# Kernel tuning notes

Measured on AMD Instinct MI355X. Metric: run time of the kernel, lower is better.

## Reference

```python
import jax, jax.numpy as jnp
import numpy as np

N = 200000      # nodes (1000 graphs x 200 nodes)
E = 1600000     # edges
N1 = 100000     # nodes after pool 1
E2 = 100000     # edges of pooled graph
N2 = 50000      # nodes after pool 2
B = 1000        # graphs
F_IN, C1, C2, H, NCLS = 1, 32, 64, 25, 10


def setup_inputs() -> dict:
    key = jax.random.key(0)
    ks = jax.random.split(key, 16)
    def lin(k, i, o):
        return jax.random.normal(k, (i, o), jnp.float32) / np.sqrt(i)
    inp = {
        'x': jax.random.normal(ks[0], (N, F_IN), jnp.float32),
        'pos': jax.random.uniform(ks[1], (N, 2), jnp.float32),
        'edge_index': jax.random.randint(ks[2], (2, E), 0, N, dtype=jnp.int32),
        'edge_attr': jax.random.uniform(ks[3], (E, 2), jnp.float32),
        'batch': (jnp.arange(N, dtype=jnp.int32) // (N // B)),
        'cluster1': (jnp.arange(N, dtype=jnp.int32) // 2),      # pairs of consecutive nodes -> same graph
        'edge_index2': jax.random.randint(ks[4], (2, E2), 0, N1, dtype=jnp.int32),
        'cluster2': (jnp.arange(N1, dtype=jnp.int32) // 2),
        'n1_w1': lin(ks[5], 2, H), 'n1_b1': jnp.zeros((H,), jnp.float32),
        'n1_w2': lin(ks[6], H, F_IN * C1), 'n1_b2': jnp.zeros((F_IN * C1,), jnp.float32),
        'root1': lin(ks[7], F_IN, C1), 'bias1': jnp.zeros((C1,), jnp.float32),
        'n2_w1': lin(ks[8], 2, H), 'n2_b1': jnp.zeros((H,), jnp.float32),
        'n2_w2': lin(ks[9], H, C1 * C2), 'n2_b2': jnp.zeros((C1 * C2,), jnp.float32),
        'root2': lin(ks[10], C1, C2), 'bias2': jnp.zeros((C2,), jnp.float32),
        'fc1_w': lin(ks[11], C2, 128), 'fc1_b': jnp.zeros((128,), jnp.float32),
        'fc2_w': lin(ks[12], 128, NCLS), 'fc2_b': jnp.zeros((NCLS,), jnp.float32),
    }
    return inp


def _cartesian(ei, pos):
    # PyG transforms.Cartesian(norm=True, cat=False)
    cart = pos[ei[0]] - pos[ei[1]]                      # [E, 2]
    m = jnp.max(jnp.abs(cart))
    return cart / (2.0 * m) + 0.5


def _nnconv(x, ei, ea, w1, b1, w2, b2, root, bias, n_nodes, c_in, c_out):
    # edge-conditioned weights: MLP(edge_attr) -> [E, c_in, c_out]
    w = (jax.nn.relu(ea @ w1 + b1) @ w2 + b2).reshape(-1, c_in, c_out)
    msg = jnp.einsum('ei,eio->eo', x[ei[0]], w)          # per-edge matmul with gathered src feats
    agg = jax.ops.segment_sum(msg, ei[1], num_segments=n_nodes)
    return agg + x @ root + bias


def _segment_mean(v, seg, n):
    s = jax.ops.segment_sum(v, seg, num_segments=n)
    c = jax.ops.segment_sum(jnp.ones((v.shape[0], 1), v.dtype), seg, num_segments=n)
    return s / jnp.maximum(c, 1.0)


def reference(x, pos, edge_index, edge_attr, batch, cluster1, edge_index2, cluster2,
              n1_w1, n1_b1, n1_w2, n1_b2, root1, bias1,
              n2_w1, n2_b1, n2_w2, n2_b2, root2, bias2,
              fc1_w, fc1_b, fc2_w, fc2_b):
    h = jax.nn.elu(_nnconv(x, edge_index, edge_attr, n1_w1, n1_b1, n1_w2, n1_b2,
                           root1, bias1, N, F_IN, C1))
    # max_pool(cluster1): segment-max feats, mean pos, carry batch; recompute Cartesian attrs
    x1 = jax.ops.segment_max(h, cluster1, num_segments=N1)
    pos1 = _segment_mean(pos, cluster1, N1)
    batch1 = jax.ops.segment_max(batch, cluster1, num_segments=N1)
    ea2 = _cartesian(edge_index2, pos1)
    h2 = jax.nn.elu(_nnconv(x1, edge_index2, ea2, n2_w1, n2_b1, n2_w2, n2_b2,
                            root2, bias2, N1, C1, C2))
    # max_pool_x(cluster2)
    x2 = jax.ops.segment_max(h2, cluster2, num_segments=N2)
    batch2 = jax.ops.segment_max(batch1, cluster2, num_segments=N2)
    g = _segment_mean(x2, batch2, B)                    # global_mean_pool -> [B, 64]
    z = jax.nn.elu(g @ fc1_w + fc1_b)                   # dropout is identity in eval
    return jax.nn.log_softmax(z @ fc2_w + fc2_b, axis=1)
```

## Files before the change

kernel.cpp:

```cpp
#include <hip/hip_runtime.h>
#include <hip/hip_bf16.h>

#define N_NODES 200000
#define E1 1600000
#define N1P 100000
#define E2P 100000
#define N2P 50000
#define BGR 1000
#define C1 32
#define C2 64
#define HIDN 25
#define NCLS 10

typedef short short8 __attribute__((ext_vector_type(8)));
typedef int int4v __attribute__((ext_vector_type(4)));
typedef float f32x4 __attribute__((ext_vector_type(4)));
typedef float f32x2 __attribute__((ext_vector_type(2)));

union FragU { int4v i; short8 s; };

__device__ __forceinline__ float elu1(float v) {
    return v > 0.f ? v : expm1f(v);
}
__device__ __forceinline__ float bf2f(unsigned short u) {
    return __uint_as_float(((unsigned int)u) << 16);
}
__device__ __forceinline__ unsigned int pk_bf16(float a, float b) {
    unsigned int r;
    asm("v_cvt_pk_bf16_f32 %0, %1, %2" : "=v"(r) : "v"(a), "v"(b));
    return r;
}
__device__ __forceinline__ void atomic_pk_bf16(unsigned short* p, unsigned int pk) {
    asm volatile("global_atomic_pk_add_bf16 %0, %1, off" :: "v"(p), "v"(pk) : "memory");
}

__global__ __launch_bounds__(256) void bgbuild1_kernel(
    const float* __restrict__ w2, const float* __restrict__ b2,
    unsigned int* __restrict__ W2f)
{
    int q = blockIdx.x * 256 + threadIdx.x;
    if (q >= 512) return;
    int jj = q & 3, l = (q >> 2) & 63, m = q >> 8;
    int k0 = (l >> 4) * 8 + 2 * jj;
    int o = 2 * (l & 15) + m;
    float v0 = (k0 < 25) ? w2[k0 * 32 + o] : (k0 == 25 ? b2[o] : 0.f);
    int k1 = k0 + 1;
    float v1 = (k1 < 25) ? w2[k1 * 32 + o] : (k1 == 25 ? b2[o] : 0.f);
    W2f[q] = pk_bf16(v0, v1);
}

__global__ __launch_bounds__(256) void conv1_kernel(
    const float* __restrict__ x, const float* __restrict__ ea,
    const int* __restrict__ ei,
    const float* __restrict__ w1, const float* __restrict__ b1,
    const unsigned int* __restrict__ W2f,
    unsigned short* __restrict__ agg1b)
{
    __shared__ unsigned int afrag[16][4][64];
    __shared__ int dst_lds[256];

    int t = threadIdx.x;
    int e = blockIdx.x * 256 + t;
    f32x2 a = ((const f32x2*)ea)[e];
    int s = ei[e], d = ei[E1 + e];
    float xv = x[s];
    dst_lds[t] = d;

    float v[26];
#pragma unroll
    for (int h = 0; h < HIDN; ++h) {
        float u = fmaf(a.x, w1[h], fmaf(a.y, w1[HIDN + h], b1[h]));
        v[h] = fmaxf(u, 0.f) * xv;
    }
    v[25] = xv;

    int tile = t >> 4, r = t & 15;
#pragma unroll
    for (int p = 0; p < 13; ++p) {
        int g = p >> 2, j = p & 3;
        afrag[tile][j][g * 16 + r] = pk_bf16(v[2 * p], v[2 * p + 1]);
    }
    afrag[tile][1][48 + r] = 0;
    afrag[tile][2][48 + r] = 0;
    afrag[tile][3][48 + r] = 0;
    __syncthreads();

    int lane = t & 63, wave = t >> 6;
    FragU bf0, bf1;
    bf0.i = *(const int4v*)(W2f + lane * 4);
    bf1.i = *(const int4v*)(W2f + (64 + lane) * 4);
    int c = lane & 15, rg = lane >> 4;

#pragma unroll
    for (int ti = 0; ti < 4; ++ti) {
        int tl = wave * 4 + ti;
        FragU af;
        af.i.x = afrag[tl][0][lane];
        af.i.y = afrag[tl][1][lane];
        af.i.z = afrag[tl][2][lane];
        af.i.w = afrag[tl][3][lane];
        f32x4 a0 = (f32x4){0.f, 0.f, 0.f, 0.f};
        f32x4 a1 = (f32x4){0.f, 0.f, 0.f, 0.f};
        a0 = __builtin_amdgcn_mfma_f32_16x16x32_bf16(af.s, bf0.s, a0, 0, 0, 0);
        a1 = __builtin_amdgcn_mfma_f32_16x16x32_bf16(af.s, bf1.s, a1, 0, 0, 0);
#pragma unroll
        for (int jj = 0; jj < 4; ++jj) {
            int le = tl * 16 + rg * 4 + jj;
            atomic_pk_bf16(agg1b + (size_t)dst_lds[le] * C1 + 2 * c,
                           pk_bf16(a0[jj], a1[jj]));
        }
    }
}

__global__ __launch_bounds__(256) void pool1_kernel(
    const unsigned short* __restrict__ agg1b, const float* __restrict__ x,
    const float* __restrict__ root1, const float* __restrict__ bias1,
    const float* __restrict__ pos, unsigned short* __restrict__ x1b,
    float* __restrict__ pos1)
{
    int t = blockIdx.x * blockDim.x + threadIdx.x;
    if (t >= N1P * C1) return;
    int j = t >> 5, o = t & 31;
    int na = 2 * j, nb = 2 * j + 1;
    float r = root1[o], bo = bias1[o];
    float ha = elu1(bf2f(agg1b[(size_t)na * C1 + o]) + x[na] * r + bo);
    float hb = elu1(bf2f(agg1b[(size_t)nb * C1 + o]) + x[nb] * r + bo);
    float mx = fmaxf(ha, hb);
    x1b[t] = (unsigned short)(pk_bf16(mx, mx) & 0xffffu);
    if (o < 2) pos1[j * 2 + o] = 0.5f * (pos[na * 2 + o] + pos[nb * 2 + o]);
}

__global__ __launch_bounds__(256) void maxabs_kernel(
    const int* __restrict__ ei2, const float* __restrict__ pos1,
    unsigned int* __restrict__ maxbits)
{
    int e = blockIdx.x * blockDim.x + threadIdx.x;
    float m = 0.f;
    if (e < E2P) {
        int s = ei2[e], d = ei2[E2P + e];
        float c0 = pos1[2 * s] - pos1[2 * d];
        float c1 = pos1[2 * s + 1] - pos1[2 * d + 1];
        m = fmaxf(fabsf(c0), fabsf(c1));
    }
#pragma unroll
    for (int off = 32; off; off >>= 1)
        m = fmaxf(m, __shfl_down(m, off));
    if ((threadIdx.x & 63) == 0)
        atomicMax(maxbits, __float_as_uint(m));
}

__global__ __launch_bounds__(256) void bgbuild_kernel(
    const float* __restrict__ w2, const float* __restrict__ b2,
    unsigned int* __restrict__ Bg)
{
    int idx = blockIdx.x * 256 + threadIdx.x;
    if (idx >= 26 * 4 * 64 * 4) return;
    int g0 = idx * 2;
    int j = g0 & 7;
    int l = (g0 >> 3) & 63;
    int nb = (g0 >> 9) & 3;
    int kt = g0 >> 11;
    int k = kt * 32 + (l >> 4) * 8 + j;
    int o = (nb >> 1) * 32 + 2 * (l & 15) + (nb & 1);
    float v0, v1;
    if (k < 800) { v0 = w2[k * 64 + o]; v1 = w2[(k + 1) * 64 + o]; }
    else         { v0 = b2[(k - 800) * 64 + o]; v1 = b2[(k - 799) * 64 + o]; }
    Bg[idx] = pk_bf16(v0, v1);
}

__global__ __launch_bounds__(256) void conv2_kernel(
    const int* __restrict__ ei2, const float* __restrict__ pos1,
    const unsigned short* __restrict__ x1b,
    const float* __restrict__ w1, const float* __restrict__ b1,
    const unsigned int* __restrict__ maxbits,
    const unsigned int* __restrict__ Bg,
    unsigned short* __restrict__ agg2b)
{
    __shared__ __align__(16) unsigned short xs_lds[256][40];
    __shared__ float hid_lds[256][27];
    __shared__ int dst_lds[256];

    int t = threadIdx.x;
    int ge = blockIdx.x * 256 + t;

    {
        float inv = 0.5f / __uint_as_float(maxbits[0]);
        int s = 0, d = 0;
        if (ge < E2P) { s = ei2[ge]; d = ei2[E2P + ge]; }
        dst_lds[t] = d;
        float a0 = (pos1[2 * s] - pos1[2 * d]) * inv + 0.5f;
        float a1 = (pos1[2 * s + 1] - pos1[2 * d + 1]) * inv + 0.5f;
#pragma unroll
        for (int h = 0; h < HIDN; ++h) {
            float u = fmaf(a0, w1[h], fmaf(a1, w1[HIDN + h], b1[h]));
            hid_lds[t][h] = fmaxf(u, 0.f);
        }
        const int4v* xp = (const int4v*)(x1b + (size_t)s * C1);
#pragma unroll
        for (int q = 0; q < 4; ++q)
            *(int4v*)&xs_lds[t][q * 8] = xp[q];
    }
    __syncthreads();

    int lane = t & 63, wave = t >> 6;
    int c = lane & 15, rg = lane >> 4;

    FragU xv4[4];
    float xfl[4][8];
#pragma unroll
    for (int ti = 0; ti < 4; ++ti) {
        int row = (wave * 4 + ti) * 16 + c;
        xv4[ti].i = *(const int4v*)&xs_lds[row][rg * 8];
#pragma unroll
        for (int g2 = 0; g2 < 4; ++g2) {
            unsigned int u = (unsigned int)xv4[ti].i[g2];
            xfl[ti][2 * g2]     = __uint_as_float(u << 16);
            xfl[ti][2 * g2 + 1] = __uint_as_float(u & 0xffff0000u);
        }
    }

    f32x4 acc[4][4];
#pragma unroll
    for (int ti = 0; ti < 4; ++ti)
#pragma unroll
        for (int nb = 0; nb < 4; ++nb)
            acc[ti][nb] = (f32x4){0.f, 0.f, 0.f, 0.f};

    const int4v* Bg4 = (const int4v*)Bg;
#pragma unroll 2
    for (int kt = 0; kt < 25; ++kt) {
        FragU bf[4];
#pragma unroll
        for (int nb = 0; nb < 4; ++nb)
            bf[nb].i = Bg4[(kt * 4 + nb) * 64 + lane];
#pragma unroll
        for (int ti = 0; ti < 4; ++ti) {
            float hv = hid_lds[(wave * 4 + ti) * 16 + c][kt];
            FragU af;
            af.i.x = pk_bf16(hv * xfl[ti][0], hv * xfl[ti][1]);
            af.i.y = pk_bf16(hv * xfl[ti][2], hv * xfl[ti][3]);
            af.i.z = pk_bf16(hv * xfl[ti][4], hv * xfl[ti][5]);
            af.i.w = pk_bf16(hv * xfl[ti][6], hv * xfl[ti][7]);
#pragma unroll
            for (int nb = 0; nb < 4; ++nb)
                acc[ti][nb] = __builtin_amdgcn_mfma_f32_16x16x32_bf16(af.s, bf[nb].s, acc[ti][nb], 0, 0, 0);
        }
    }
    {
        FragU bf[4];
#pragma unroll
        for (int nb = 0; nb < 4; ++nb)
            bf[nb].i = Bg4[(25 * 4 + nb) * 64 + lane];
#pragma unroll
        for (int ti = 0; ti < 4; ++ti)
#pragma unroll
            for (int nb = 0; nb < 4; ++nb)
                acc[ti][nb] = __builtin_amdgcn_mfma_f32_16x16x32_bf16(xv4[ti].s, bf[nb].s, acc[ti][nb], 0, 0, 0);
    }

#pragma unroll
    for (int ti = 0; ti < 4; ++ti) {
        int tl = wave * 4 + ti;
#pragma unroll
        for (int jj = 0; jj < 4; ++jj) {
            int le = tl * 16 + rg * 4 + jj;
            if (blockIdx.x * 256 + le < E2P) {
                unsigned short* dp = agg2b + (size_t)dst_lds[le] * C2;
                atomic_pk_bf16(dp + 2 * c,      pk_bf16(acc[ti][0][jj], acc[ti][1][jj]));
                atomic_pk_bf16(dp + 32 + 2 * c, pk_bf16(acc[ti][2][jj], acc[ti][3][jj]));
            }
        }
    }
}

__global__ __launch_bounds__(256) void pool2_kernel(
    const unsigned short* __restrict__ agg2b, const unsigned short* __restrict__ x1b,
    const float* __restrict__ root2, const float* __restrict__ bias2,
    float* __restrict__ g)
{
    int b = blockIdx.x;
    int w = threadIdx.x >> 6, o = threadIdx.x & 63;
    __shared__ float part[4][C2];
    float sum = 0.f;
    for (int jj = w; jj < 50; jj += 4) {
        int j = b * 50 + jj;
        float hv[2];
#pragma unroll
        for (int t = 0; t < 2; ++t) {
            int n = 2 * j + t;
            float a = bf2f(agg2b[(size_t)n * C2 + o]) + bias2[o];
#pragma unroll
            for (int i = 0; i < C1; ++i)
                a = fmaf(bf2f(x1b[(size_t)n * C1 + i]), root2[i * C2 + o], a);
            hv[t] = elu1(a);
        }
        sum += fmaxf(hv[0], hv[1]);
    }
    part[w][o] = sum;
    __syncthreads();
    if (w == 0) {
        float s2 = part[0][o] + part[1][o] + part[2][o] + part[3][o];
        g[b * C2 + o] = s2 * (1.f / 50.f);
    }
}

__global__ __launch_bounds__(128) void head_kernel(
    const float* __restrict__ g,
    const float* __restrict__ fc1w, const float* __restrict__ fc1b,
    const float* __restrict__ fc2w, const float* __restrict__ fc2b,
    float* __restrict__ out)
{
    int b = blockIdx.x;
    int t = threadIdx.x;
    __shared__ float gs[C2];
    __shared__ float zs[128];
    __shared__ float ls[NCLS];
    if (t < C2) gs[t] = g[b * C2 + t];
    __syncthreads();
    float z = fc1b[t];
#pragma unroll
    for (int i = 0; i < C2; ++i) z = fmaf(gs[i], fc1w[i * 128 + t], z);
    zs[t] = elu1(z);
    __syncthreads();
    if (t < NCLS) {
        float l = fc2b[t];
#pragma unroll
        for (int k = 0; k < 128; ++k) l = fmaf(zs[k], fc2w[k * NCLS + t], l);
        ls[t] = l;
    }
    __syncthreads();
    if (t < NCLS) {
        float mx = ls[0];
#pragma unroll
        for (int c = 1; c < NCLS; ++c) mx = fmaxf(mx, ls[c]);
        float se = 0.f;
#pragma unroll
        for (int c = 0; c < NCLS; ++c) se += expf(ls[c] - mx);
        out[b * NCLS + t] = ls[t] - mx - logf(se);
    }
}

extern "C" void kernel_launch(void* const* d_in, const int* in_sizes, int n_in,
                              void* d_out, int out_size, void* d_ws, size_t ws_size,
                              hipStream_t stream)
{
    const float* x    = (const float*)d_in[0];
    const float* pos  = (const float*)d_in[1];
    const int*   ei   = (const int*)d_in[2];
    const float* ea   = (const float*)d_in[3];
    const int*   ei2  = (const int*)d_in[6];
    const float* n1w1 = (const float*)d_in[8];
    const float* n1b1 = (const float*)d_in[9];
    const float* n1w2 = (const float*)d_in[10];
    const float* n1b2 = (const float*)d_in[11];
    const float* root1= (const float*)d_in[12];
    const float* bias1= (const float*)d_in[13];
    const float* n2w1 = (const float*)d_in[14];
    const float* n2b1 = (const float*)d_in[15];
    const float* n2w2 = (const float*)d_in[16];
    const float* n2b2 = (const float*)d_in[17];
    const float* root2= (const float*)d_in[18];
    const float* bias2= (const float*)d_in[19];
    const float* fc1w = (const float*)d_in[20];
    const float* fc1b = (const float*)d_in[21];
    const float* fc2w = (const float*)d_in[22];
    const float* fc2b = (const float*)d_in[23];
    float* out = (float*)d_out;

    char* w = (char*)d_ws;
    unsigned short* agg1b = (unsigned short*)w;  w += (size_t)N_NODES * C1 * 2;
    unsigned short* x1b   = (unsigned short*)w;  w += (size_t)N1P * C1 * 2;
    float* pos1 = (float*)w;                     w += (size_t)N1P * 2 * 4;
    unsigned int* maxbits = (unsigned int*)w;    w += 256;
    unsigned short* agg2b = (unsigned short*)w;  w += (size_t)N1P * C2 * 2;
    float* g    = (float*)w;                     w += (size_t)BGR * C2 * 4;
    unsigned int* Bg = (unsigned int*)w;         w += 26624 * 4;
    unsigned int* W2f = (unsigned int*)w;        w += 512 * 4;

    hipMemsetAsync(agg1b, 0, (size_t)N_NODES * C1 * 2, stream);
    hipMemsetAsync(agg2b, 0, (size_t)N1P * C2 * 2, stream);
    hipMemsetAsync(maxbits, 0, 256, stream);

    bgbuild1_kernel<<<2, 256, 0, stream>>>(n1w2, n1b2, W2f);
    bgbuild_kernel<<<104, 256, 0, stream>>>(n2w2, n2b2, Bg);
    conv1_kernel<<<E1 / 256, 256, 0, stream>>>(x, ea, ei, n1w1, n1b1, W2f, agg1b);
    pool1_kernel<<<(N1P * C1 + 255) / 256, 256, 0, stream>>>(agg1b, x, root1, bias1, pos, x1b, pos1);
    maxabs_kernel<<<(E2P + 255) / 256, 256, 0, stream>>>(ei2, pos1, maxbits);
    conv2_kernel<<<(E2P + 255) / 256, 256, 0, stream>>>(ei2, pos1, x1b, n2w1, n2b1, maxbits, Bg, agg2b);
    pool2_kernel<<<BGR, 256, 0, stream>>>(agg2b, x1b, root2, bias2, g);
    head_kernel<<<BGR, 128, 0, stream>>>(g, fc1w, fc1b, fc2w, fc2b, out);
}
```

Before: 188.1 us.

## Sort conv1 edges by destination and reduce runs in LDS before scattering

Adds a counting sort of edges by destination (histogram, single-block scan, atomic scatter) so conv1 processes destination-sorted edges. Messages are staged in LDS, contiguous runs with the same destination are summed in fp32, and each run is written once, with a plain store for interior runs and an atomic only at block boundaries. This cuts the roughly 1.6M packed-bf16 atomics, but adds three kernels, extra memsets, gather-indirect loads of edge_attr and src, and a serial single-block scan over 200k counts.

```diff
diff --git a/kernel.cpp b/kernel.cpp
--- a/kernel.cpp
+++ b/kernel.cpp
@@ -11,6 +11,7 @@
 #define C2 64
 #define HIDN 25
 #define NCLS 10
+#define SCAN_CHUNK 196
 
 typedef short short8 __attribute__((ext_vector_type(8)));
 typedef int int4v __attribute__((ext_vector_type(4)));
@@ -32,6 +33,52 @@
 }
 __device__ __forceinline__ void atomic_pk_bf16(unsigned short* p, unsigned int pk) {
     asm volatile("global_atomic_pk_add_bf16 %0, %1, off" :: "v"(p), "v"(pk) : "memory");
+}
+
+__global__ __launch_bounds__(256) void hist_kernel(
+    const int* __restrict__ ei, int* __restrict__ cnt)
+{
+    int e = blockIdx.x * 256 + threadIdx.x;
+    if (e < E1) atomicAdd(&cnt[ei[E1 + e]], 1);
+}
+
+__global__ __launch_bounds__(1024) void scan_kernel(
+    const int* __restrict__ cnt, int* __restrict__ offs)
+{
+    __shared__ int ssum[1024];
+    int t = threadIdx.x;
+    int base = t * SCAN_CHUNK;
+    int s = 0;
+    for (int i = 0; i < SCAN_CHUNK; ++i) {
+        int idx = base + i;
+        s += (idx < N_NODES) ? cnt[idx] : 0;
+    }
+    ssum[t] = s;
+    __syncthreads();
+    for (int off = 1; off < 1024; off <<= 1) {
+        int v = (t >= off) ? ssum[t - off] : 0;
+        __syncthreads();
+        ssum[t] += v;
+        __syncthreads();
+    }
+    int run = (t == 0) ? 0 : ssum[t - 1];
+    for (int i = 0; i < SCAN_CHUNK; ++i) {
+        int idx = base + i;
+        if (idx < N_NODES) { offs[idx] = run; run += cnt[idx]; }
+    }
+}
+
+__global__ __launch_bounds__(256) void scatter_kernel(
+    const int* __restrict__ ei, const int* __restrict__ offs,
+    int* __restrict__ cur, int* __restrict__ sorted_eid, int* __restrict__ sorted_dst)
+{
+    int e = blockIdx.x * 256 + threadIdx.x;
+    if (e >= E1) return;
+    int d = ei[E1 + e];
+    int r = atomicAdd(&cur[d], 1);
+    int slot = offs[d] + r;
+    sorted_eid[slot] = e;
+    sorted_dst[slot] = d;
 }
 
 __global__ __launch_bounds__(256) void bgbuild1_kernel(
@@ -54,17 +101,28 @@
     const int* __restrict__ ei,
     const float* __restrict__ w1, const float* __restrict__ b1,
     const unsigned int* __restrict__ W2f,
+    const int* __restrict__ sorted_eid, const int* __restrict__ sorted_dst,
     unsigned short* __restrict__ agg1b)
 {
     __shared__ unsigned int afrag[16][4][64];
-    __shared__ int dst_lds[256];
+    __shared__ unsigned int msg_lds[256][17];
+    __shared__ int dst_lds[258];
+    __shared__ int runstart[260];
+    __shared__ int wave_cnt[4];
+    __shared__ int nruns;
 
     int t = threadIdx.x;
-    int e = blockIdx.x * 256 + t;
-    f32x2 a = ((const f32x2*)ea)[e];
-    int s = ei[e], d = ei[E1 + e];
+    int base = blockIdx.x * 256;
+    int slot = base + t;
+    int eid = sorted_eid[slot];
+    int d = sorted_dst[slot];
+    dst_lds[t] = d;
+    if (t == 0) dst_lds[256] = (base > 0) ? sorted_dst[base - 1] : -1;
+    if (t == 1) dst_lds[257] = (base + 256 < E1) ? sorted_dst[base + 256] : -1;
+
+    f32x2 a = ((const f32x2*)ea)[eid];
+    int s = ei[eid];
     float xv = x[s];
-    dst_lds[t] = d;
 
     float v[26];
 #pragma unroll
@@ -74,15 +132,15 @@
     }
     v[25] = xv;
 
-    int tile = t >> 4, r = t & 15;
+    int tile = t >> 4, r16 = t & 15;
 #pragma unroll
     for (int p = 0; p < 13; ++p) {
         int g = p >> 2, j = p & 3;
-        afrag[tile][j][g * 16 + r] = pk_bf16(v[2 * p], v[2 * p + 1]);
-    }
-    afrag[tile][1][48 + r] = 0;
-    afrag[tile][2][48 + r] = 0;
-    afrag[tile][3][48 + r] = 0;
+        afrag[tile][j][g * 16 + r16] = pk_bf16(v[2 * p], v[2 * p + 1]);
+    }
+    afrag[tile][1][48 + r16] = 0;
+    afrag[tile][2][48 + r16] = 0;
+    afrag[tile][3][48 + r16] = 0;
     __syncthreads();
 
     int lane = t & 63, wave = t >> 6;
@@ -104,11 +162,43 @@
         a0 = __builtin_amdgcn_mfma_f32_16x16x32_bf16(af.s, bf0.s, a0, 0, 0, 0);
         a1 = __builtin_amdgcn_mfma_f32_16x16x32_bf16(af.s, bf1.s, a1, 0, 0, 0);
 #pragma unroll
-        for (int jj = 0; jj < 4; ++jj) {
-            int le = tl * 16 + rg * 4 + jj;
-            atomic_pk_bf16(agg1b + (size_t)dst_lds[le] * C1 + 2 * c,
-                           pk_bf16(a0[jj], a1[jj]));
-        }
+        for (int jj = 0; jj < 4; ++jj)
+            msg_lds[tl * 16 + rg * 4 + jj][c] = pk_bf16(a0[jj], a1[jj]);
+    }
+    __syncthreads();
+
+    int prevd = (t == 0) ? -2 : dst_lds[t - 1];
+    bool flag = (t == 0) || (d != prevd);
+    unsigned long long mask = __ballot(flag);
+    int ln = lane;
+    if (ln == 0) wave_cnt[wave] = __popcll(mask);
+    __syncthreads();
+    int wbase = 0;
+    for (int i = 0; i < wave; ++i) wbase += wave_cnt[i];
+    if (flag)
+        runstart[wbase + __popcll(mask & ((1ull << ln) - 1ull))] = t;
+    if (t == 0) {
+        int R = wave_cnt[0] + wave_cnt[1] + wave_cnt[2] + wave_cnt[3];
+        nruns = R;
+        runstart[R] = 256;
+    }
+    __syncthreads();
+    int R = nruns;
+
+    int grp = t >> 4, gl = t & 15;
+    for (int r = grp; r < R; r += 16) {
+        int st = runstart[r], en = runstart[r + 1];
+        int rd = dst_lds[st];
+        float s0 = 0.f, s1 = 0.f;
+        for (int i = st; i < en; ++i) {
+            unsigned int u = msg_lds[i][gl];
+            s0 += __uint_as_float(u << 16);
+            s1 += __uint_as_float(u & 0xffff0000u);
+        }
+        bool open = (r == 0 && rd == dst_lds[256]) || (r == R - 1 && rd == dst_lds[257]);
+        unsigned short* p = agg1b + (size_t)rd * C1 + 2 * gl;
+        if (open) atomic_pk_bf16(p, pk_bf16(s0, s1));
+        else      *(unsigned int*)p = pk_bf16(s0, s1);
     }
 }
 
@@ -376,14 +466,25 @@
     float* g    = (float*)w;                     w += (size_t)BGR * C2 * 4;
     unsigned int* Bg = (unsigned int*)w;         w += 26624 * 4;
     unsigned int* W2f = (unsigned int*)w;        w += 512 * 4;
+    int* cnt  = (int*)w;                         w += (size_t)N_NODES * 4;
+    int* offs = (int*)w;                         w += (size_t)N_NODES * 4;
+    int* cur  = (int*)w;                         w += (size_t)N_NODES * 4;
+    int* sorted_eid = (int*)w;                   w += (size_t)E1 * 4;
+    int* sorted_dst = (int*)w;                   w += (size_t)E1 * 4;
 
     hipMemsetAsync(agg1b, 0, (size_t)N_NODES * C1 * 2, stream);
     hipMemsetAsync(agg2b, 0, (size_t)N1P * C2 * 2, stream);
     hipMemsetAsync(maxbits, 0, 256, stream);
+    hipMemsetAsync(cnt, 0, (size_t)N_NODES * 4, stream);
+    hipMemsetAsync(cur, 0, (size_t)N_NODES * 4, stream);
 
     bgbuild1_kernel<<<2, 256, 0, stream>>>(n1w2, n1b2, W2f);
     bgbuild_kernel<<<104, 256, 0, stream>>>(n2w2, n2b2, Bg);
-    conv1_kernel<<<E1 / 256, 256, 0, stream>>>(x, ea, ei, n1w1, n1b1, W2f, agg1b);
+    hist_kernel<<<E1 / 256, 256, 0, stream>>>(ei, cnt);
+    scan_kernel<<<1, 1024, 0, stream>>>(cnt, offs);
+    scatter_kernel<<<E1 / 256, 256, 0, stream>>>(ei, offs, cur, sorted_eid, sorted_dst);
+    conv1_kernel<<<E1 / 256, 256, 0, stream>>>(x, ea, ei, n1w1, n1b1, W2f,
+                                               sorted_eid, sorted_dst, agg1b);
     pool1_kernel<<<(N1P * C1 + 255) / 256, 256, 0, stream>>>(agg1b, x, root1, bias1, pos, x1b, pos1);
     maxabs_kernel<<<(E2P + 255) / 256, 256, 0, stream>>>(ei2, pos1, maxbits);
     conv2_kernel<<<(E2P + 255) / 256, 256, 0, stream>>>(ei2, pos1, x1b, n2w1, n2b1, maxbits, Bg, agg2b);
```

After: 715.9 us. 280% more time.
